# Kernel optimization log

Hardware: AMD Instinct MI355X
Metric: run time of the kernel (lower is better)

## Reference

```python
import jax, jax.numpy as jnp
import numpy as np

LAMB = 1.0
EPS = 1e-16


def setup_inputs() -> dict:
    key = jax.random.key(0)
    kx, km = jax.random.split(key)
    N, D, K = 262144, 128, 64
    x = jax.random.normal(kx, (N, D), dtype=jnp.float32)
    m = jax.random.normal(km, (K, D), dtype=jnp.float32)
    m = m / jnp.linalg.norm(m, axis=1, keepdims=True)  # unit-norm rows like __init__
    return {"x": x, "m": m}


def _entropy(p):
    # replicate torch.where clamping
    p = jnp.where(p <= 0, EPS, p)
    p = jnp.where(p >= 1, 1.0 - EPS, p)
    return -jnp.sum(p * jnp.log(p), axis=-1)


def _p(x, m):
    d2 = (jnp.sum(x * x, axis=-1, keepdims=True)
          - 2.0 * x @ m.T
          + jnp.sum(m * m, axis=-1))  # [N, K]
    return jax.nn.softmax(-d2, axis=-1)


def reference(x, m):
    p = _p(x, m)                      # [N, K]
    intra = jnp.mean(_entropy(p))     # scalar
    mu = jnp.mean(m, axis=0)          # [D]
    p_inter = _p(mu[None, :], m)[0]   # [K]
    inter = _entropy(p_inter)
    total = intra - LAMB * inter
    return (total, intra, inter)
```

## Files before the change

### kernel.cpp

```cpp
#include <hip/hip_runtime.h>

#define D 128
#define K 64

typedef __attribute__((ext_vector_type(8))) short short8;
typedef __attribute__((ext_vector_type(2))) int int2v;
typedef __attribute__((ext_vector_type(4))) float f32x4;

__device__ inline short f2bf(float f) {
  union { float f; unsigned u; } v; v.f = f;
  unsigned u = v.u;
  return (short)((u + 0x7fffu + ((u >> 16) & 1u)) >> 16);
}

__device__ inline int cvt_pk_bf16(float lo, float hi) {
  int r;
  asm("v_cvt_pk_bf16_f32 %0, %1, %2" : "=v"(r) : "v"(lo), "v"(hi));
  return r;
}

template<int CTRL>
__device__ inline float dpp_ror(float x) {
  return __builtin_bit_cast(float, __builtin_amdgcn_update_dpp(
      0, __builtin_bit_cast(int, x), CTRL, 0xF, 0xF, true));
}
__device__ inline float rowsum16(float v) {
  v += dpp_ror<0x121>(v);
  v += dpp_ror<0x122>(v);
  v += dpp_ror<0x124>(v);
  v += dpp_ror<0x128>(v);
  return v;
}
__device__ inline float rowmax16(float v) {
  v = fmaxf(v, dpp_ror<0x121>(v));
  v = fmaxf(v, dpp_ror<0x122>(v));
  v = fmaxf(v, dpp_ror<0x124>(v));
  v = fmaxf(v, dpp_ror<0x128>(v));
  return v;
}

#define LOADX(dst, t) do {                                                  \
    const f32x4* xb = (const f32x4*)(x + (size_t)(t) * (16 * D)) + lane;    \
    _Pragma("unroll") for (int p = 0; p < 8; ++p) dst[p] = xb[p * 64];      \
  } while (0)

#define PACKX(src) do {                                                     \
    _Pragma("unroll") for (int p = 0; p < 8; ++p) {                         \
      f32x4 v = src[p];                                                     \
      int2v s;                                                              \
      s[0] = cvt_pk_bf16(v[0], v[1]);                                       \
      s[1] = cvt_pk_bf16(v[2], v[3]);                                       \
      int r = 2 * p + hi;                                                   \
      *(int2v*)(amem + r * 256 + ((wc ^ r) << 4) + wh * 8) = s;             \
    }                                                                       \
  } while (0)

#define TILE_COMPUTE() do {                                                 \
    f32x4 acc[4];                                                           \
    _Pragma("unroll") for (int jt = 0; jt < 4; ++jt)                        \
      acc[jt] = (f32x4){0.f, 0.f, 0.f, 0.f};                                \
    _Pragma("unroll") for (int kk = 0; kk < 4; ++kk) {                      \
      short8 afrag = *(const short8*)(amem + ra[kk]);                       \
      _Pragma("unroll") for (int jt = 0; jt < 4; ++jt)                      \
        acc[jt] = __builtin_amdgcn_mfma_f32_16x16x32_bf16(                  \
            afrag, bsm[cbase[kk] + jt * 256], acc[jt], 0, 0, 0);            \
    }                                                                       \
    _Pragma("unroll") for (int r = 0; r < 4; ++r) {                         \
      float s0 = acc[0][r] - mn[0];                                         \
      float s1 = acc[1][r] - mn[1];                                         \
      float s2 = acc[2][r] - mn[2];                                         \
      float s3 = acc[3][r] - mn[3];                                         \
      float mx = rowmax16(fmaxf(fmaxf(s0, s1), fmaxf(s2, s3)));             \
      float t0 = s0 - mx, t1 = s1 - mx, t2 = s2 - mx, t3 = s3 - mx;         \
      float e0 = __expf(t0), e1 = __expf(t1);                               \
      float e2 = __expf(t2), e3 = __expf(t3);                               \
      float S0 = rowsum16((e0 + e1) + (e2 + e3));                           \
      float S1 = rowsum16((t0 * e0 + t1 * e1) + (t2 * e2 + t3 * e3));       \
      float H = __logf(S0) - S1 / S0;                                       \
      hacc += (lid == 0) ? H : 0.0f;                                        \
    }                                                                       \
  } while (0)

__launch_bounds__(256, 2)
__global__ void main_kernel(const float* __restrict__ x, const float* __restrict__ m,
                            float* ws, int nTiles, int totalWaves) {
  __shared__ short8 bsm[1024];
  __shared__ float mnorms[K];
  __shared__ char asmem[4][4096];

  const int tid = threadIdx.x;
  for (int i = tid; i < K * D; i += 256) {
    int c = i >> 3, e = i & 7;
    int cs = c ^ ((c >> 4) & 7);
    ((short*)bsm)[cs * 8 + e] = f2bf(2.0f * m[i]);
  }
  if (tid < K) {
    const float* mr = m + tid * D;
    float s = 0.f;
    for (int d = 0; d < D; ++d) s += mr[d] * mr[d];
    mnorms[tid] = s;
  }
  __syncthreads();

  const int lane = tid & 63;
  const int lid  = lane & 15;
  const int quad = lane >> 4;
  const int wid  = tid >> 6;
  char* amem = asmem[wid];

  float mn[4];
#pragma unroll
  for (int jt = 0; jt < 4; ++jt) mn[jt] = mnorms[jt * 16 + lid];

  int cbase[4], ra[4];
#pragma unroll
  for (int kk = 0; kk < 4; ++kk) {
    cbase[kk] = (lid * 16 + kk * 4 + quad) ^ (lid & 7);
    ra[kk] = lid * 256 + ((((kk << 2) | quad) ^ lid) << 4);
  }

  const int hi = lane >> 5;
  const int wc = (lane & 31) >> 1;
  const int wh = lane & 1;

  const int wave = blockIdx.x * 4 + wid;
  float hacc = 0.f;

  f32x4 ld0[8], ld1[8], ld2[8], ld3[8];
  const int t0 = wave;
  const int t1 = wave + totalWaves;
  const int t2 = wave + 2 * totalWaves;
  const int t3 = wave + 3 * totalWaves;
  LOADX(ld0, t0);
  if (t1 < nTiles) LOADX(ld1, t1);
  if (t2 < nTiles) LOADX(ld2, t2);
  if (t3 < nTiles) LOADX(ld3, t3);

  PACKX(ld0); TILE_COMPUTE();
  if (t1 < nTiles) { PACKX(ld1); TILE_COMPUTE(); }
  if (t2 < nTiles) { PACKX(ld2); TILE_COMPUTE(); }
  if (t3 < nTiles) { PACKX(ld3); TILE_COMPUTE(); }

  for (int off = 1; off < 64; off <<= 1) hacc += __shfl_xor(hacc, off, 64);
  __shared__ float red[4];
  if (lane == 0) red[wid] = hacc;
  __syncthreads();
  if (tid == 0) ws[blockIdx.x] = red[0] + red[1] + red[2] + red[3];
}

__global__ void final_kernel(const float* __restrict__ m, const float* ws, float* out,
                             int nRows, int nBlocks) {
  __shared__ float mu[D];
  int lane = threadIdx.x;
  for (int d = lane; d < D; d += 64) {
    float s = 0.f;
    for (int j = 0; j < K; ++j) s += m[j * D + d];
    mu[d] = s * (1.0f / K);
  }
  __syncthreads();

  float part = 0.f;
  for (int i = lane; i < nBlocks; i += 64) part += ws[i];
  for (int off = 1; off < 64; off <<= 1) part += __shfl_xor(part, off, 64);

  const float* mr = m + lane * D;
  float dot = 0.f, nrm = 0.f;
  for (int d = 0; d < D; ++d) {
    dot += mu[d] * mr[d];
    nrm += mr[d] * mr[d];
  }
  float s = 2.f * dot - nrm;
  float mx = s;
  for (int off = 1; off < 64; off <<= 1) mx = fmaxf(mx, __shfl_xor(mx, off, 64));
  float t = s - mx;
  float e = __expf(t);
  float S0 = e, S1 = t * e;
  for (int off = 1; off < 64; off <<= 1) {
    S0 += __shfl_xor(S0, off, 64);
    S1 += __shfl_xor(S1, off, 64);
  }
  float inter = __logf(S0) - S1 / S0;
  if (lane == 0) {
    float intra = part / (float)nRows;
    out[0] = intra - inter;
    out[1] = intra;
    out[2] = inter;
  }
}

extern "C" void kernel_launch(void* const* d_in, const int* in_sizes, int n_in,
                              void* d_out, int out_size, void* d_ws, size_t ws_size,
                              hipStream_t stream) {
  const float* x = (const float*)d_in[0];
  const float* m = (const float*)d_in[1];
  float* ws = (float*)d_ws;
  float* out = (float*)d_out;
  const int N = in_sizes[0] / D;
  const int nTiles = N / 16;

  const int blocks = 1024;
  const int totalWaves = blocks * 4;
  main_kernel<<<blocks, 256, 0, stream>>>(x, m, ws, nTiles, totalWaves);

  final_kernel<<<1, 64, 0, stream>>>(m, ws, out, N, blocks);
}
```

Baseline: 201.8 us.

## Halve grid, software-pipeline x loads over eight tiles, vectorize m staging

Halves the block count so each wave handles eight 16-row tiles instead of four. Each register buffer is refilled with its next tile right after being packed to LDS, so global loads overlap the MFMA/softmax work of earlier tiles. The m-to-bf16 staging and the norm computation now use float4 loads and packed conversion. Bounds checks are removed, so the kernel assumes N is exactly 512*4*8*16 rows (it was already hardcoded to the test shape). The trade-off is fewer blocks to amortize per-block setup and higher register pressure.

```diff
diff --git a/kernel.cpp b/kernel.cpp
--- a/kernel.cpp
+++ b/kernel.cpp
@@ -6,12 +6,6 @@
 typedef __attribute__((ext_vector_type(8))) short short8;
 typedef __attribute__((ext_vector_type(2))) int int2v;
 typedef __attribute__((ext_vector_type(4))) float f32x4;
-
-__device__ inline short f2bf(float f) {
-  union { float f; unsigned u; } v; v.f = f;
-  unsigned u = v.u;
-  return (short)((u + 0x7fffu + ((u >> 16) & 1u)) >> 16);
-}
 
 __device__ inline int cvt_pk_bf16(float lo, float hi) {
   int r;
@@ -83,21 +77,33 @@
 
 __launch_bounds__(256, 2)
 __global__ void main_kernel(const float* __restrict__ x, const float* __restrict__ m,
-                            float* ws, int nTiles, int totalWaves) {
+                            float* ws, int totalWaves) {
   __shared__ short8 bsm[1024];
   __shared__ float mnorms[K];
   __shared__ char asmem[4][4096];
 
   const int tid = threadIdx.x;
-  for (int i = tid; i < K * D; i += 256) {
-    int c = i >> 3, e = i & 7;
+
+  const f32x4* mv4 = (const f32x4*)m;
+#pragma unroll
+  for (int i0 = 0; i0 < (K * D) / 4; i0 += 256) {
+    int i = i0 + tid;
+    f32x4 v = mv4[i];
+    int c = i >> 1, h = i & 1;
     int cs = c ^ ((c >> 4) & 7);
-    ((short*)bsm)[cs * 8 + e] = f2bf(2.0f * m[i]);
+    int2v s;
+    s[0] = cvt_pk_bf16(2.f * v[0], 2.f * v[1]);
+    s[1] = cvt_pk_bf16(2.f * v[2], 2.f * v[3]);
+    *(int2v*)((char*)bsm + cs * 16 + h * 8) = s;
   }
   if (tid < K) {
-    const float* mr = m + tid * D;
+    const f32x4* mr = (const f32x4*)(m + tid * D);
     float s = 0.f;
-    for (int d = 0; d < D; ++d) s += mr[d] * mr[d];
+#pragma unroll
+    for (int i = 0; i < 32; ++i) {
+      f32x4 v = mr[i];
+      s += (v[0] * v[0] + v[1] * v[1]) + (v[2] * v[2] + v[3] * v[3]);
+    }
     mnorms[tid] = s;
   }
   __syncthreads();
@@ -124,22 +130,23 @@
   const int wh = lane & 1;
 
   const int wave = blockIdx.x * 4 + wid;
+  const int W = totalWaves;
   float hacc = 0.f;
 
   f32x4 ld0[8], ld1[8], ld2[8], ld3[8];
-  const int t0 = wave;
-  const int t1 = wave + totalWaves;
-  const int t2 = wave + 2 * totalWaves;
-  const int t3 = wave + 3 * totalWaves;
-  LOADX(ld0, t0);
-  if (t1 < nTiles) LOADX(ld1, t1);
-  if (t2 < nTiles) LOADX(ld2, t2);
-  if (t3 < nTiles) LOADX(ld3, t3);
-
+  LOADX(ld0, wave);
+  LOADX(ld1, wave + W);
+  LOADX(ld2, wave + 2 * W);
+  LOADX(ld3, wave + 3 * W);
+
+  PACKX(ld0); LOADX(ld0, wave + 4 * W); TILE_COMPUTE();
+  PACKX(ld1); LOADX(ld1, wave + 5 * W); TILE_COMPUTE();
+  PACKX(ld2); LOADX(ld2, wave + 6 * W); TILE_COMPUTE();
+  PACKX(ld3); LOADX(ld3, wave + 7 * W); TILE_COMPUTE();
   PACKX(ld0); TILE_COMPUTE();
-  if (t1 < nTiles) { PACKX(ld1); TILE_COMPUTE(); }
-  if (t2 < nTiles) { PACKX(ld2); TILE_COMPUTE(); }
-  if (t3 < nTiles) { PACKX(ld3); TILE_COMPUTE(); }
+  PACKX(ld1); TILE_COMPUTE();
+  PACKX(ld2); TILE_COMPUTE();
+  PACKX(ld3); TILE_COMPUTE();
 
   for (int off = 1; off < 64; off <<= 1) hacc += __shfl_xor(hacc, off, 64);
   __shared__ float red[4];
@@ -196,11 +203,10 @@
   float* ws = (float*)d_ws;
   float* out = (float*)d_out;
   const int N = in_sizes[0] / D;
-  const int nTiles = N / 16;
-
-  const int blocks = 1024;
+
+  const int blocks = 512;
   const int totalWaves = blocks * 4;
-  main_kernel<<<blocks, 256, 0, stream>>>(x, m, ws, nTiles, totalWaves);
+  main_kernel<<<blocks, 256, 0, stream>>>(x, m, ws, totalWaves);
 
   final_kernel<<<1, 64, 0, stream>>>(m, ws, out, N, blocks);
 }
```

After: 198.2 us. No clear change (-1.8%).
